# Kernel tuning notes

Hardware: AMD Instinct MI355X
Metric: run time of the kernel (lower is better)

The kernel has to match this reference:

```python
import jax, jax.numpy as jnp
import numpy as np

B, S, D, H, W, L, V = 4, 8192, 256, 8, 64, 6, 256
DH = D // H          # head dim 32
NW = S // W          # number of windows
FF = 4 * D


def setup_inputs() -> dict:
    key = jax.random.key(0)
    ks = jax.random.split(key, 12)
    w = lambda k, shape: (jax.random.normal(k, shape, jnp.float32) * 0.02)
    return {
        "input_ids": jax.random.randint(ks[0], (B, S), 0, V).astype(jnp.int32),
        "attention_mask": jnp.ones((B, S), jnp.int32),
        "word_start": jax.random.randint(ks[1], (B, S), 0, 2).astype(jnp.int32),
        "emb": w(ks[2], (V, D)),
        "pos_emb": w(ks[3], (S, D)),
        "ln1_g": jnp.ones((L, D)), "ln1_b": jnp.zeros((L, D)),
        "wq": w(ks[4], (L, D, D)), "wk": w(ks[5], (L, D, D)),
        "wv": w(ks[6], (L, D, D)), "wo": w(ks[7], (L, D, D)),
        "ln2_g": jnp.ones((L, D)), "ln2_b": jnp.zeros((L, D)),
        "w1": w(ks[8], (L, D, FF)), "b1": jnp.zeros((L, FF)),
        "w2": w(ks[9], (L, FF, D)), "b2": jnp.zeros((L, D)),
        "lnf_g": jnp.ones((D,)), "lnf_b": jnp.zeros((D,)),
    }


def _ln(x, g, b):
    m = jnp.mean(x, -1, keepdims=True)
    v = jnp.mean((x - m) ** 2, -1, keepdims=True)
    return (x - m) * jax.lax.rsqrt(v + 1e-5) * g + b


def _local_attn(x, mask_bool, wq, wk, wv, wo):
    # non-causal local attention: each 64-token window attends to
    # [prev window, own window, next window] (look_backward=1, look_forward=1)
    def heads(t):
        return t.reshape(B, S, H, DH).transpose(0, 2, 1, 3)  # [B,H,S,DH]
    q = heads(x @ wq)
    k = heads(x @ wk)
    v = heads(x @ wv)
    qw = q.reshape(B, H, NW, W, DH)

    def ctx(t):  # gather 3-window key/value context
        tw = t.reshape(B, H, NW, W, DH)
        tp = jnp.pad(tw, ((0, 0), (0, 0), (1, 1), (0, 0), (0, 0)))
        return jnp.concatenate([tp[:, :, i:i + NW] for i in range(3)], axis=3)  # [B,H,NW,3W,DH]

    kc, vc = ctx(k), ctx(v)
    mw = mask_bool.reshape(B, NW, W)
    mp = jnp.pad(mw, ((0, 0), (1, 1), (0, 0)))
    mc = jnp.concatenate([mp[:, i:i + NW] for i in range(3)], axis=2)  # [B,NW,3W]

    scores = jnp.einsum('bhnwd,bhnkd->bhnwk', qw, kc) * (DH ** -0.5)
    scores = jnp.where(mc[:, None, :, None, :], scores, -1e9)
    attn = jax.nn.softmax(scores, axis=-1)
    o = jnp.einsum('bhnwk,bhnkd->bhnwd', attn, vc)
    o = o.reshape(B, H, S, DH).transpose(0, 2, 1, 3).reshape(B, S, D)
    return o @ wo


def _gather_word_starts(x, ws):
    # pack hidden states at word-start positions to the front, zero-padded
    def one(xb, wb):
        idx = jnp.cumsum(wb) - 1
        tgt = jnp.where(wb > 0, idx, S)  # invalid rows go to scratch slot S
        return jnp.zeros((S + 1, xb.shape[-1]), xb.dtype).at[tgt].set(xb)[:S]
    return jax.vmap(one)(x, ws)


def reference(input_ids, attention_mask, word_start, emb, pos_emb,
              ln1_g, ln1_b, wq, wk, wv, wo, ln2_g, ln2_b,
              w1, b1, w2, b2, lnf_g, lnf_b):
    mask_bool = attention_mask > 0
    x = emb[input_ids] + pos_emb[None, :, :]
    for i in range(L):
        x = x + _local_attn(_ln(x, ln1_g[i], ln1_b[i]), mask_bool,
                            wq[i], wk[i], wv[i], wo[i])
        h = _ln(x, ln2_g[i], ln2_b[i])
        x = x + jax.nn.gelu(h @ w1[i] + b1[i]) @ w2[i] + b2[i]
    x = _ln(x, lnf_g, lnf_b)
    return _gather_word_starts(x, word_start)
```

## Files before the change

### kernel.cpp

```cpp
#include <hip/hip_runtime.h>


#define S_LEN 8192
#define BATCH 4
#define DMODEL 256
#define NHEAD 8
#define WIN 64
#define NWIN 128
#define NLAYER 6
#define FFDIM 1024
#define MROWS (BATCH * S_LEN)

typedef float __attribute__((ext_vector_type(4))) f32x4;
typedef unsigned int __attribute__((ext_vector_type(2))) u32x2;
typedef unsigned short u16;
typedef unsigned short __attribute__((ext_vector_type(4))) u16x4;

__device__ __forceinline__ u16 f2bf(float f) {
  unsigned u = __builtin_bit_cast(unsigned, f);
  u += 0x7fffu + ((u >> 16) & 1u);
  return (u16)(u >> 16);
}

__device__ __forceinline__ unsigned cvt_pk_bf16(float lo, float hi) {
  unsigned r;
  asm("v_cvt_pk_bf16_f32 %0, %1, %2" : "=v"(r) : "v"(lo), "v"(hi));
  return r;
}
__device__ __forceinline__ u32x2 pack_bf16x4(f32x4 v) {
  u32x2 o;
  o[0] = cvt_pk_bf16(v[0], v[1]);
  o[1] = cvt_pk_bf16(v[2], v[3]);
  return o;
}

__device__ __forceinline__ void mfma16(f32x4& d, f32x4 a, f32x4 b) {
  asm volatile("v_mfma_f32_16x16x32_bf16 %0, %1, %2, %0"
               : "+v"(d) : "v"(a), "v"(b));
}
#define MFMA_FENCE() asm volatile("s_nop 7\n\ts_nop 7")

__device__ __forceinline__ void gload_lds16(const void* g, void* l) {
  __builtin_amdgcn_global_load_lds(
      (__attribute__((address_space(1))) void*)g,
      (__attribute__((address_space(3))) void*)l, 16, 0, 0);
}

__device__ __forceinline__ float gelu_f(float t) {
  float u = 0.7978845608028654f * (t + 0.044715f * t * t * t);
  float e = __expf(-2.0f * u);
  return t * __builtin_amdgcn_rcpf(1.0f + e);
}

__global__ __launch_bounds__(256) void embed_ln_kernel(
    const int* __restrict__ ids, const float* __restrict__ emb,
    const float* __restrict__ pos, const float* __restrict__ g,
    const float* __restrict__ b, float* __restrict__ x, u16* __restrict__ xb) {
  int wid = threadIdx.x >> 6, lane = threadIdx.x & 63;
  int r = blockIdx.x * 4 + wid;
  int s = r & (S_LEN - 1);
  int id = ids[r];
  f32x4 e = *(const f32x4*)(emb + (size_t)id * DMODEL + lane * 4);
  f32x4 p = *(const f32x4*)(pos + (size_t)s * DMODEL + lane * 4);
  f32x4 v = e + p;
  *(f32x4*)(x + (size_t)r * DMODEL + lane * 4) = v;
  float sm = v[0] + v[1] + v[2] + v[3];
  float q = v[0] * v[0] + v[1] * v[1] + v[2] * v[2] + v[3] * v[3];
  for (int off = 32; off; off >>= 1) {
    sm += __shfl_xor(sm, off, 64);
    q += __shfl_xor(q, off, 64);
  }
  float mean = sm * (1.0f / DMODEL);
  float var = q * (1.0f / DMODEL) - mean * mean;
  float rs = rsqrtf(var + 1e-5f);
  f32x4 gg = *(const f32x4*)(g + lane * 4);
  f32x4 bb = *(const f32x4*)(b + lane * 4);
  f32x4 o;
  for (int j = 0; j < 4; ++j) o[j] = (v[j] - mean) * rs * gg[j] + bb[j];
  *(u32x2*)(xb + (size_t)r * DMODEL + lane * 4) = pack_bf16x4(o);
}

__global__ void zero_kernel(float* __restrict__ p, int n4) {
  int i = blockIdx.x * blockDim.x + threadIdx.x;
  int stride = gridDim.x * blockDim.x;
  f32x4 z = {0.f, 0.f, 0.f, 0.f};
  for (; i < n4; i += stride) ((f32x4*)p)[i] = z;
}

__global__ void tcast_kernel(const float* __restrict__ src, u16* __restrict__ dst,
                             int total, int K, int N, int dls, int rowOff) {
  int i = blockIdx.x * blockDim.x + threadIdx.x;
  int stride = gridDim.x * blockDim.x;
  int KN = K * N;
  for (; i < total; i += stride) {
    int l = i / KN;
    int rem = i - l * KN;
    int k = rem / N;
    int n = rem - k * N;
    dst[l * dls + (rowOff + n) * K + k] = f2bf(src[i]);
  }
}

template <bool GELU_ACT, bool HAS_BIAS>
__global__ __launch_bounds__(256) void gemm_bf16(
    const u16* __restrict__ A, const u16* __restrict__ Bt,
    u16* __restrict__ C, const float* __restrict__ bias,
    int N, int K, int nx) {
  __shared__ u16 As[128 * 64];
  __shared__ u16 Bs[128 * 64];

  int nwg = gridDim.x;
  int bid = blockIdx.x;
  int w8 = (bid & 7) * (nwg >> 3) + (bid >> 3);
  int cx = w8 % nx, ry = w8 / nx;
  int bm = ry * 128, bn = cx * 128;

  int tid = threadIdx.x, lane = tid & 63, wid = tid >> 6;
  int l15 = lane & 15, l4 = lane >> 4;
  int wm = wid >> 1, wn = wid & 1;

  const u16* Ab = A + (size_t)bm * K;
  const u16* Bb = Bt + (size_t)bn * K;

  f32x4 acc[4][4] = {};

  for (int kt = 0; kt < K; kt += 64) {
#pragma unroll
    for (int i = 0; i < 4; ++i) {
      int s = tid + i * 256;
      int r = s >> 3, c = (s & 7) ^ (r & 7);
      gload_lds16(Ab + (size_t)r * K + kt + c * 8,
                  (char*)As + (wid * 64 + i * 256) * 16);
    }
#pragma unroll
    for (int i = 0; i < 4; ++i) {
      int s = tid + i * 256;
      int r = s >> 3, c = (s & 7) ^ (r & 7);
      gload_lds16(Bb + (size_t)r * K + kt + c * 8,
                  (char*)Bs + (wid * 64 + i * 256) * 16);
    }
    __syncthreads();
#pragma unroll
    for (int t = 0; t < 2; ++t) {
      f32x4 af[4], bf[4];
#pragma unroll
      for (int m = 0; m < 4; ++m) {
        int r = wm * 64 + m * 16 + l15;
        af[m] = ((const f32x4*)As)[r * 8 + ((t * 4 + l4) ^ (r & 7))];
      }
#pragma unroll
      for (int n = 0; n < 4; ++n) {
        int r = wn * 64 + n * 16 + l15;
        bf[n] = ((const f32x4*)Bs)[r * 8 + ((t * 4 + l4) ^ (r & 7))];
      }
#pragma unroll
      for (int m = 0; m < 4; ++m)
#pragma unroll
        for (int n = 0; n < 4; ++n) mfma16(acc[m][n], bf[n], af[m]);
    }
    __syncthreads();
  }
  MFMA_FENCE();

  int colB = bn + wn * 64;
  f32x4 bv[4];
#pragma unroll
  for (int n = 0; n < 4; ++n)
    bv[n] = HAS_BIAS ? *(const f32x4*)(bias + colB + n * 16 + l4 * 4)
                     : (f32x4){0.f, 0.f, 0.f, 0.f};
#pragma unroll
  for (int m = 0; m < 4; ++m) {
    int row = bm + wm * 64 + m * 16 + l15;
#pragma unroll
    for (int n = 0; n < 4; ++n) {
      f32x4 v = acc[m][n] + bv[n];
      if (GELU_ACT) {
#pragma unroll
        for (int j = 0; j < 4; ++j) v[j] = gelu_f(v[j]);
      }
      *(u32x2*)(C + (size_t)row * N + colB + n * 16 + l4 * 4) = pack_bf16x4(v);
    }
  }
}

template <bool DO_LN>
__global__ __launch_bounds__(512) void gemm_res_ln(
    const u16* __restrict__ A, const u16* __restrict__ Bt,
    float* __restrict__ x, u16* __restrict__ xb,
    const float* __restrict__ bias, const float* __restrict__ g,
    const float* __restrict__ b, int K) {
  __shared__ u16 As[128 * 64];
  __shared__ u16 Bs[256 * 64];
  __shared__ float redS[128][4];
  __shared__ float redQ[128][4];

  int nwg = gridDim.x;
  int bid = blockIdx.x;
  int bm = ((bid & 7) * (nwg >> 3) + (bid >> 3)) * 128;

  int tid = threadIdx.x, lane = tid & 63, wid = tid >> 6;
  int l15 = lane & 15, l4 = lane >> 4;
  int wm = wid >> 2, wn = wid & 3;

  const u16* Ab = A + (size_t)bm * K;
  f32x4 acc[4][4] = {};

  for (int kt = 0; kt < K; kt += 64) {
#pragma unroll
    for (int i = 0; i < 2; ++i) {
      int s = tid + i * 512;
      int r = s >> 3, c = (s & 7) ^ (r & 7);
      gload_lds16(Ab + (size_t)r * K + kt + c * 8,
                  (char*)As + (wid * 64 + i * 512) * 16);
    }
#pragma unroll
    for (int i = 0; i < 4; ++i) {
      int s = tid + i * 512;
      int r = s >> 3, c = (s & 7) ^ (r & 7);
      gload_lds16(Bt + (size_t)r * K + kt + c * 8,
                  (char*)Bs + (wid * 64 + i * 512) * 16);
    }
    __syncthreads();
#pragma unroll
    for (int t = 0; t < 2; ++t) {
      f32x4 af[4], bf[4];
#pragma unroll
      for (int m = 0; m < 4; ++m) {
        int r = wm * 64 + m * 16 + l15;
        af[m] = ((const f32x4*)As)[r * 8 + ((t * 4 + l4) ^ (r & 7))];
      }
#pragma unroll
      for (int n = 0; n < 4; ++n) {
        int r = wn * 64 + n * 16 + l15;
        bf[n] = ((const f32x4*)Bs)[r * 8 + ((t * 4 + l4) ^ (r & 7))];
      }
#pragma unroll
      for (int m = 0; m < 4; ++m)
#pragma unroll
        for (int n = 0; n < 4; ++n) mfma16(acc[m][n], bf[n], af[m]);
    }
    __syncthreads();
  }
  MFMA_FENCE();

  int colB = wn * 64;
  f32x4 bv[4];
#pragma unroll
  for (int n = 0; n < 4; ++n)
    bv[n] = bias ? *(const f32x4*)(bias + colB + n * 16 + l4 * 4)
                 : (f32x4){0.f, 0.f, 0.f, 0.f};

#pragma unroll
  for (int m = 0; m < 4; ++m) {
    int r = wm * 64 + m * 16 + l15;
    size_t rowoff = (size_t)(bm + r) * DMODEL + colB;
    float s = 0.f, q = 0.f;
#pragma unroll
    for (int n = 0; n < 4; ++n) {
      f32x4 xv = *(const f32x4*)(x + rowoff + n * 16 + l4 * 4);
      f32x4 v = acc[m][n] + bv[n] + xv;
      acc[m][n] = v;
      s += v[0] + v[1] + v[2] + v[3];
      q += v[0] * v[0] + v[1] * v[1] + v[2] * v[2] + v[3] * v[3];
    }
    if (DO_LN) {
      s += __shfl_xor(s, 16, 64);
      s += __shfl_xor(s, 32, 64);
      q += __shfl_xor(q, 16, 64);
      q += __shfl_xor(q, 32, 64);
      if (l4 == 0) {
        redS[r][wn] = s;
        redQ[r][wn] = q;
      }
    }
  }
  if (DO_LN) __syncthreads();

  f32x4 gv[4], bbv[4];
  if (DO_LN) {
#pragma unroll
    for (int n = 0; n < 4; ++n) {
      gv[n] = *(const f32x4*)(g + colB + n * 16 + l4 * 4);
      bbv[n] = *(const f32x4*)(b + colB + n * 16 + l4 * 4);
    }
  }
#pragma unroll
  for (int m = 0; m < 4; ++m) {
    int r = wm * 64 + m * 16 + l15;
    size_t rowoff = (size_t)(bm + r) * DMODEL + colB;
    float mean = 0.f, rs = 0.f;
    if (DO_LN) {
      f32x4 sv = *(const f32x4*)redS[r];
      f32x4 qv = *(const f32x4*)redQ[r];
      float ssum = sv[0] + sv[1] + sv[2] + sv[3];
      float qsum = qv[0] + qv[1] + qv[2] + qv[3];
      mean = ssum * (1.0f / DMODEL);
      float var = qsum * (1.0f / DMODEL) - mean * mean;
      rs = rsqrtf(var + 1e-5f);
    }
#pragma unroll
    for (int n = 0; n < 4; ++n) {
      f32x4 v = acc[m][n];
      *(f32x4*)(x + rowoff + n * 16 + l4 * 4) = v;
      if (DO_LN) {
        f32x4 o;
#pragma unroll
        for (int j = 0; j < 4; ++j)
          o[j] = (v[j] - mean) * rs * gv[n][j] + bbv[n][j];
        *(u32x2*)(xb + rowoff + n * 16 + l4 * 4) = pack_bf16x4(o);
      }
    }
  }
}

__global__ __launch_bounds__(256, 4) void attn_kernel(
    const u16* __restrict__ qkv, const int* __restrict__ amask,
    u16* __restrict__ ao) {
  int win = blockIdx.x, h = blockIdx.y, b = blockIdx.z;
  int tid = threadIdx.x, lane = tid & 63, wid = tid >> 6;
  int l15 = lane & 15, l4 = lane >> 4;

  __shared__ u16 KPs[64 * 216];
  __shared__ u16 Vts[32 * 200];
  __shared__ unsigned char valid[192];

  int t0 = win * WIN - WIN;

  if (tid < 192) {
    int t = t0 + tid;
    valid[tid] = (t >= 0 && t < S_LEN && amask[b * S_LEN + t] != 0) ? 1 : 0;
  }
#pragma unroll
  for (int cc = 0; cc < 3; ++cc) {
    int chunk = cc * 256 + tid;
    int key = chunk >> 2, c = chunk & 3;
    int t = t0 + key;
    t = t < 0 ? 0 : (t >= S_LEN ? S_LEN - 1 : t);
    f32x4 kd = *(const f32x4*)(qkv + (size_t)(b * S_LEN + t) * 768 + 256 + h * 32 + c * 8);
    *(f32x4*)(KPs + key * 40 + c * 8) = kd;
  }
  for (int e = tid; e < 192 * 32; e += 256) {
    int key = e >> 5, d = e & 31;
    int t = t0 + key;
    t = t < 0 ? 0 : (t >= S_LEN ? S_LEN - 1 : t);
    Vts[d * 200 + key] = qkv[(size_t)(b * S_LEN + t) * 768 + 512 + h * 32 + d];
  }
  __syncthreads();

  int qrow = b * S_LEN + win * WIN + wid * 16 + l15;
  f32x4 aq = *(const f32x4*)(qkv + (size_t)qrow * 768 + h * 32 + l4 * 8);

  f32x4 sacc[12] = {};
#pragma unroll
  for (int f = 0; f < 12; ++f) {
    f32x4 bk = *(const f32x4*)(KPs + (f * 16 + l15) * 40 + l4 * 8);
    mfma16(sacc[f], bk, aq);
  }
  MFMA_FENCE();

  const float scale = 0.17677669529663687f;
  float mrow = -1e30f;
#pragma unroll
  for (int f = 0; f < 12; ++f) {
    const unsigned char* vp = &valid[f * 16 + l4 * 4];
#pragma unroll
    for (int j = 0; j < 4; ++j) {
      float sv = vp[j] ? sacc[f][j] * scale : -1e9f;
      sacc[f][j] = sv;
      mrow = fmaxf(mrow, sv);
    }
  }
  mrow = fmaxf(mrow, __shfl_xor(mrow, 16, 64));
  mrow = fmaxf(mrow, __shfl_xor(mrow, 32, 64));

  float ssum = 0.f;
#pragma unroll
  for (int f = 0; f < 12; ++f)
#pragma unroll
    for (int j = 0; j < 4; ++j) {
      float p = __expf(sacc[f][j] - mrow);
      sacc[f][j] = p;
      ssum += p;
    }
  ssum += __shfl_xor(ssum, 16, 64);
  ssum += __shfl_xor(ssum, 32, 64);

  __syncthreads();

#pragma unroll
  for (int f = 0; f < 12; ++f) {
    u32x2 pk;
    pk[0] = cvt_pk_bf16(sacc[f][0], sacc[f][1]);
    pk[1] = cvt_pk_bf16(sacc[f][2], sacc[f][3]);
    *(u32x2*)(KPs + (wid * 16 + l15) * 216 + f * 16 + l4 * 4) = pk;
  }
  __syncthreads();

  f32x4 oacc[2] = {};
#pragma unroll
  for (int kk = 0; kk < 6; ++kk) {
    f32x4 ap = *(const f32x4*)(KPs + (wid * 16 + l15) * 216 + kk * 32 + l4 * 8);
#pragma unroll
    for (int nf = 0; nf < 2; ++nf) {
      f32x4 bvv = *(const f32x4*)(Vts + (nf * 16 + l15) * 200 + kk * 32 + l4 * 8);
      mfma16(oacc[nf], bvv, ap);
    }
  }
  MFMA_FENCE();

  float invv = 1.0f / ssum;
  size_t obase = (size_t)qrow * 256 + h * 32;
#pragma unroll
  for (int nf = 0; nf < 2; ++nf) {
    f32x4 v = oacc[nf] * invv;
    *(u32x2*)(ao + obase + nf * 16 + l4 * 4) = pack_bf16x4(v);
  }
}

__global__ __launch_bounds__(256) void scan_kernel(const int* __restrict__ wsrt,
                                                   int* __restrict__ tgt) {
  __shared__ int part[256];
  int b = blockIdx.x, tid = threadIdx.x;
  const int* src = wsrt + b * S_LEN;
  int* dst = tgt + b * S_LEN;
  int base = tid * 32;
  int loc[32];
  int s = 0;
#pragma unroll
  for (int i = 0; i < 32; ++i) {
    loc[i] = src[base + i];
    s += loc[i];
  }
  part[tid] = s;
  __syncthreads();
  for (int off = 1; off < 256; off <<= 1) {
    int v = (tid >= off) ? part[tid - off] : 0;
    __syncthreads();
    part[tid] += v;
    __syncthreads();
  }
  int cum = part[tid] - s;
#pragma unroll
  for (int i = 0; i < 32; ++i) {
    cum += loc[i];
    dst[base + i] = (loc[i] > 0) ? (cum - 1) : -1;
  }
}

__global__ __launch_bounds__(64) void gather_ln_kernel(
    const float* __restrict__ x, const int* __restrict__ tgt,
    const float* __restrict__ g, const float* __restrict__ b,
    float* __restrict__ out) {
  int r = blockIdx.x;
  int tg = tgt[r];
  if (tg < 0) return;
  int bIdx = r >> 13;
  int lane = threadIdx.x;
  f32x4 v = *(const f32x4*)(x + (size_t)r * DMODEL + lane * 4);
  float s = v[0] + v[1] + v[2] + v[3];
  float q = v[0] * v[0] + v[1] * v[1] + v[2] * v[2] + v[3] * v[3];
  for (int off = 32; off; off >>= 1) {
    s += __shfl_xor(s, off, 64);
    q += __shfl_xor(q, off, 64);
  }
  float mean = s * (1.0f / DMODEL);
  float var = q * (1.0f / DMODEL) - mean * mean;
  float rs = rsqrtf(var + 1e-5f);
  f32x4 gg = *(const f32x4*)(g + lane * 4);
  f32x4 bb = *(const f32x4*)(b + lane * 4);
  f32x4 o;
  for (int j = 0; j < 4; ++j) o[j] = (v[j] - mean) * rs * gg[j] + bb[j];
  *(f32x4*)(out + (size_t)(bIdx * S_LEN + tg) * DMODEL + lane * 4) = o;
}

extern "C" void kernel_launch(void* const* d_in, const int* in_sizes, int n_in,
                              void* d_out, int out_size, void* d_ws,
                              size_t ws_size, hipStream_t stream) {
  const int* ids = (const int*)d_in[0];
  const int* amask = (const int*)d_in[1];
  const int* wstart = (const int*)d_in[2];
  const float* emb = (const float*)d_in[3];
  const float* pos = (const float*)d_in[4];
  const float* ln1g = (const float*)d_in[5];
  const float* ln1b = (const float*)d_in[6];
  const float* wq = (const float*)d_in[7];
  const float* wk = (const float*)d_in[8];
  const float* wv = (const float*)d_in[9];
  const float* wo = (const float*)d_in[10];
  const float* ln2g = (const float*)d_in[11];
  const float* ln2b = (const float*)d_in[12];
  const float* w1 = (const float*)d_in[13];
  const float* b1 = (const float*)d_in[14];
  const float* w2 = (const float*)d_in[15];
  const float* b2 = (const float*)d_in[16];
  const float* lnfg = (const float*)d_in[17];
  const float* lnfb = (const float*)d_in[18];

  char* ws = (char*)d_ws;
  const size_t OFF_X = 0;
  const size_t OFF_XB = 33554432;
  const size_t OFF_AO = 50331648;
  const size_t OFF_BIG = 67108864;
  const size_t OFF_WQKVT = 134217728;
  const size_t OFF_WOT = 136577024;
  const size_t OFF_W1T = 137363456;
  const size_t OFF_W2T = 140509184;
  const size_t OFF_TGT = 143654912;
  const size_t NEEDED = 143785984;
  if (ws_size < NEEDED) return;

  float* x = (float*)(ws + OFF_X);
  u16* xb = (u16*)(ws + OFF_XB);
  u16* ao = (u16*)(ws + OFF_AO);
  u16* big = (u16*)(ws + OFF_BIG);
  u16* WqkvT = (u16*)(ws + OFF_WQKVT);
  u16* WoT = (u16*)(ws + OFF_WOT);
  u16* W1T = (u16*)(ws + OFF_W1T);
  u16* W2T = (u16*)(ws + OFF_W2T);
  int* tgt = (int*)(ws + OFF_TGT);

  tcast_kernel<<<1024, 256, 0, stream>>>(wq, WqkvT, NLAYER * 256 * 256, 256, 256, 768 * 256, 0);
  tcast_kernel<<<1024, 256, 0, stream>>>(wk, WqkvT, NLAYER * 256 * 256, 256, 256, 768 * 256, 256);
  tcast_kernel<<<1024, 256, 0, stream>>>(wv, WqkvT, NLAYER * 256 * 256, 256, 256, 768 * 256, 512);
  tcast_kernel<<<1024, 256, 0, stream>>>(wo, WoT, NLAYER * 256 * 256, 256, 256, 256 * 256, 0);
  tcast_kernel<<<2048, 256, 0, stream>>>(w1, W1T, NLAYER * 256 * 1024, 256, 1024, 1024 * 256, 0);
  tcast_kernel<<<2048, 256, 0, stream>>>(w2, W2T, NLAYER * 1024 * 256, 1024, 256, 256 * 1024, 0);

  embed_ln_kernel<<<MROWS / 4, 256, 0, stream>>>(ids, emb, pos, ln1g, ln1b, x, xb);
  zero_kernel<<<2048, 256, 0, stream>>>((float*)d_out, out_size / 4);
  scan_kernel<<<BATCH, 256, 0, stream>>>(wstart, tgt);

  for (int l = 0; l < NLAYER; ++l) {
    gemm_bf16<false, false><<<1536, 256, 0, stream>>>(
        xb, WqkvT + (size_t)l * 768 * 256, big, nullptr, 768, 256, 6);
    attn_kernel<<<dim3(NWIN, NHEAD, BATCH), 256, 0, stream>>>(big, amask, ao);
    gemm_res_ln<true><<<MROWS / 128, 512, 0, stream>>>(
        ao, WoT + (size_t)l * 256 * 256, x, xb, nullptr,
        ln2g + l * DMODEL, ln2b + l * DMODEL, 256);
    gemm_bf16<true, true><<<2048, 256, 0, stream>>>(
        xb, W1T + (size_t)l * 1024 * 256, big, b1 + l * FFDIM, 1024, 256, 8);
    if (l < NLAYER - 1) {
      gemm_res_ln<true><<<MROWS / 128, 512, 0, stream>>>(
          big, W2T + (size_t)l * 256 * 1024, x, xb, b2 + l * DMODEL,
          ln1g + (l + 1) * DMODEL, ln1b + (l + 1) * DMODEL, 1024);
    } else {
      gemm_res_ln<false><<<MROWS / 128, 512, 0, stream>>>(
          big, W2T + (size_t)l * 256 * 1024, x, nullptr, b2 + l * DMODEL,
          nullptr, nullptr, 1024);
    }
  }

  gather_ln_kernel<<<MROWS, 64, 0, stream>>>(x, tgt, lnfg, lnfb, (float*)d_out);
}
```

Before: 979.4 us.

## Double-buffer GEMM LDS tiles with BK=32 and shrink residual-LN GEMM tiles

Both GEMM kernels now use two LDS buffers with a K-step of 32. The next tile's global-to-LDS load is issued before computing on the current one, and a single vmcnt wait plus barrier replaces the two __syncthreads per iteration. A new 4-column XOR swizzle matches the narrower tile. The residual+LayerNorm GEMM moves from 128-row, 512-thread blocks to 64-row, 256-thread blocks with each wave owning 64 columns, which doubles the grid and lowers LDS per block. In exchange the K loop runs twice as many iterations, each with a barrier, and the smaller tiles reuse data less.

```diff
diff --git a/kernel.cpp b/kernel.cpp
--- a/kernel.cpp
+++ b/kernel.cpp
@@ -40,6 +40,12 @@
 }
 #define MFMA_FENCE() asm volatile("s_nop 7\n\ts_nop 7")
 
+#define PIPE_SYNC()                                      \
+  do {                                                   \
+    asm volatile("s_waitcnt vmcnt(0)" ::: "memory");     \
+    __builtin_amdgcn_s_barrier();                        \
+  } while (0)
+
 __device__ __forceinline__ void gload_lds16(const void* g, void* l) {
   __builtin_amdgcn_global_load_lds(
       (__attribute__((address_space(1))) void*)g,
@@ -51,6 +57,8 @@
   float e = __expf(-2.0f * u);
   return t * __builtin_amdgcn_rcpf(1.0f + e);
 }
+
+__device__ __forceinline__ int swz3(int r) { return (r & 3) ^ ((r >> 2) & 3); }
 
 __global__ __launch_bounds__(256) void embed_ln_kernel(
     const int* __restrict__ ids, const float* __restrict__ emb,
@@ -106,8 +114,8 @@
     const u16* __restrict__ A, const u16* __restrict__ Bt,
     u16* __restrict__ C, const float* __restrict__ bias,
     int N, int K, int nx) {
-  __shared__ u16 As[128 * 64];
-  __shared__ u16 Bs[128 * 64];
+  __shared__ u16 As[2][128 * 32];
+  __shared__ u16 Bs[2][128 * 32];
 
   int nwg = gridDim.x;
   int bid = blockIdx.x;
@@ -123,42 +131,49 @@
   const u16* Bb = Bt + (size_t)bn * K;
 
   f32x4 acc[4][4] = {};
-
-  for (int kt = 0; kt < K; kt += 64) {
-#pragma unroll
-    for (int i = 0; i < 4; ++i) {
+  int NT = K >> 5;
+
+  auto stage = [&](int buf, int kt) {
+#pragma unroll
+    for (int i = 0; i < 2; ++i) {
       int s = tid + i * 256;
-      int r = s >> 3, c = (s & 7) ^ (r & 7);
+      int r = s >> 2, c = (s & 3) ^ swz3(r);
       gload_lds16(Ab + (size_t)r * K + kt + c * 8,
-                  (char*)As + (wid * 64 + i * 256) * 16);
-    }
-#pragma unroll
-    for (int i = 0; i < 4; ++i) {
+                  (char*)As[buf] + (size_t)(i * 256 + wid * 64 + lane) * 16);
+    }
+#pragma unroll
+    for (int i = 0; i < 2; ++i) {
       int s = tid + i * 256;
-      int r = s >> 3, c = (s & 7) ^ (r & 7);
+      int r = s >> 2, c = (s & 3) ^ swz3(r);
       gload_lds16(Bb + (size_t)r * K + kt + c * 8,
-                  (char*)Bs + (wid * 64 + i * 256) * 16);
-    }
-    __syncthreads();
-#pragma unroll
-    for (int t = 0; t < 2; ++t) {
-      f32x4 af[4], bf[4];
-#pragma unroll
-      for (int m = 0; m < 4; ++m) {
-        int r = wm * 64 + m * 16 + l15;
-        af[m] = ((const f32x4*)As)[r * 8 + ((t * 4 + l4) ^ (r & 7))];
-      }
-#pragma unroll
-      for (int n = 0; n < 4; ++n) {
-        int r = wn * 64 + n * 16 + l15;
-        bf[n] = ((const f32x4*)Bs)[r * 8 + ((t * 4 + l4) ^ (r & 7))];
-      }
-#pragma unroll
-      for (int m = 0; m < 4; ++m)
-#pragma unroll
-        for (int n = 0; n < 4; ++n) mfma16(acc[m][n], bf[n], af[m]);
-    }
-    __syncthreads();
+                  (char*)Bs[buf] + (size_t)(i * 256 + wid * 64 + lane) * 16);
+    }
+  };
+
+  stage(0, 0);
+  PIPE_SYNC();
+  int cur = 0;
+  for (int it = 0; it < NT; ++it) {
+    if (it + 1 < NT) stage(cur ^ 1, (it + 1) * 32);
+    const f32x4* Ap = (const f32x4*)As[cur];
+    const f32x4* Bp = (const f32x4*)Bs[cur];
+    f32x4 af[4], bf[4];
+#pragma unroll
+    for (int m = 0; m < 4; ++m) {
+      int r = wm * 64 + m * 16 + l15;
+      af[m] = Ap[r * 4 + (l4 ^ swz3(r))];
+    }
+#pragma unroll
+    for (int n = 0; n < 4; ++n) {
+      int r = wn * 64 + n * 16 + l15;
+      bf[n] = Bp[r * 4 + (l4 ^ swz3(r))];
+    }
+#pragma unroll
+    for (int m = 0; m < 4; ++m)
+#pragma unroll
+      for (int n = 0; n < 4; ++n) mfma16(acc[m][n], bf[n], af[m]);
+    PIPE_SYNC();
+    cur ^= 1;
   }
   MFMA_FENCE();
 
@@ -184,66 +199,71 @@
 }
 
 template <bool DO_LN>
-__global__ __launch_bounds__(512) void gemm_res_ln(
+__global__ __launch_bounds__(256) void gemm_res_ln(
     const u16* __restrict__ A, const u16* __restrict__ Bt,
     float* __restrict__ x, u16* __restrict__ xb,
     const float* __restrict__ bias, const float* __restrict__ g,
     const float* __restrict__ b, int K) {
-  __shared__ u16 As[128 * 64];
-  __shared__ u16 Bs[256 * 64];
-  __shared__ float redS[128][4];
-  __shared__ float redQ[128][4];
+  __shared__ u16 As[2][64 * 32];
+  __shared__ u16 Bs[2][256 * 32];
+  __shared__ float redS[64][4];
+  __shared__ float redQ[64][4];
 
   int nwg = gridDim.x;
   int bid = blockIdx.x;
-  int bm = ((bid & 7) * (nwg >> 3) + (bid >> 3)) * 128;
+  int bm = ((bid & 7) * (nwg >> 3) + (bid >> 3)) * 64;
 
   int tid = threadIdx.x, lane = tid & 63, wid = tid >> 6;
   int l15 = lane & 15, l4 = lane >> 4;
-  int wm = wid >> 2, wn = wid & 3;
 
   const u16* Ab = A + (size_t)bm * K;
   f32x4 acc[4][4] = {};
-
-  for (int kt = 0; kt < K; kt += 64) {
-#pragma unroll
-    for (int i = 0; i < 2; ++i) {
-      int s = tid + i * 512;
-      int r = s >> 3, c = (s & 7) ^ (r & 7);
+  int NT = K >> 5;
+
+  auto stage = [&](int buf, int kt) {
+    {
+      int s = tid;
+      int r = s >> 2, c = (s & 3) ^ swz3(r);
       gload_lds16(Ab + (size_t)r * K + kt + c * 8,
-                  (char*)As + (wid * 64 + i * 512) * 16);
+                  (char*)As[buf] + (size_t)(wid * 64 + lane) * 16);
     }
 #pragma unroll
     for (int i = 0; i < 4; ++i) {
-      int s = tid + i * 512;
-      int r = s >> 3, c = (s & 7) ^ (r & 7);
+      int s = tid + i * 256;
+      int r = s >> 2, c = (s & 3) ^ swz3(r);
       gload_lds16(Bt + (size_t)r * K + kt + c * 8,
-                  (char*)Bs + (wid * 64 + i * 512) * 16);
-    }
-    __syncthreads();
-#pragma unroll
-    for (int t = 0; t < 2; ++t) {
-      f32x4 af[4], bf[4];
-#pragma unroll
-      for (int m = 0; m < 4; ++m) {
-        int r = wm * 64 + m * 16 + l15;
-        af[m] = ((const f32x4*)As)[r * 8 + ((t * 4 + l4) ^ (r & 7))];
-      }
-#pragma unroll
-      for (int n = 0; n < 4; ++n) {
-        int r = wn * 64 + n * 16 + l15;
-        bf[n] = ((const f32x4*)Bs)[r * 8 + ((t * 4 + l4) ^ (r & 7))];
-      }
-#pragma unroll
-      for (int m = 0; m < 4; ++m)
-#pragma unroll
-        for (int n = 0; n < 4; ++n) mfma16(acc[m][n], bf[n], af[m]);
-    }
-    __syncthreads();
+                  (char*)Bs[buf] + (size_t)(i * 256 + wid * 64 + lane) * 16);
+    }
+  };
+
+  stage(0, 0);
+  PIPE_SYNC();
+  int cur = 0;
+  for (int it = 0; it < NT; ++it) {
+    if (it + 1 < NT) stage(cur ^ 1, (it + 1) * 32);
+    const f32x4* Ap = (const f32x4*)As[cur];
+    const f32x4* Bp = (const f32x4*)Bs[cur];
+    f32x4 af[4], bf[4];
+#pragma unroll
+    for (int m = 0; m < 4; ++m) {
+      int r = m * 16 + l15;
+      af[m] = Ap[r * 4 + (l4 ^ swz3(r))];
+    }
+#pragma unroll
+    for (int n = 0; n < 4; ++n) {
+      int r = wid * 64 + n * 16 + l15;
+      bf[n] = Bp[r * 4 + (l4 ^ swz3(r))];
+    }
+#pragma unroll
+    for (int m = 0; m < 4; ++m)
+#pragma unroll
+      for (int n = 0; n < 4; ++n) mfma16(acc[m][n], bf[n], af[m]);
+    PIPE_SYNC();
+    cur ^= 1;
   }
   MFMA_FENCE();
 
-  int colB = wn * 64;
+  int colB = wid * 64;
   f32x4 bv[4];
 #pragma unroll
   for (int n = 0; n < 4; ++n)
@@ -252,7 +272,7 @@
 
 #pragma unroll
   for (int m = 0; m < 4; ++m) {
-    int r = wm * 64 + m * 16 + l15;
+    int r = m * 16 + l15;
     size_t rowoff = (size_t)(bm + r) * DMODEL + colB;
     float s = 0.f, q = 0.f;
 #pragma unroll
@@ -269,8 +289,8 @@
       q += __shfl_xor(q, 16, 64);
       q += __shfl_xor(q, 32, 64);
       if (l4 == 0) {
-        redS[r][wn] = s;
-        redQ[r][wn] = q;
+        redS[r][wid] = s;
+        redQ[r][wid] = q;
       }
     }
   }
@@ -286,7 +306,7 @@
   }
 #pragma unroll
   for (int m = 0; m < 4; ++m) {
-    int r = wm * 64 + m * 16 + l15;
+    int r = m * 16 + l15;
     size_t rowoff = (size_t)(bm + r) * DMODEL + colB;
     float mean = 0.f, rs = 0.f;
     if (DO_LN) {
@@ -534,17 +554,17 @@
     gemm_bf16<false, false><<<1536, 256, 0, stream>>>(
         xb, WqkvT + (size_t)l * 768 * 256, big, nullptr, 768, 256, 6);
     attn_kernel<<<dim3(NWIN, NHEAD, BATCH), 256, 0, stream>>>(big, amask, ao);
-    gemm_res_ln<true><<<MROWS / 128, 512, 0, stream>>>(
+    gemm_res_ln<true><<<MROWS / 64, 256, 0, stream>>>(
         ao, WoT + (size_t)l * 256 * 256, x, xb, nullptr,
         ln2g + l * DMODEL, ln2b + l * DMODEL, 256);
     gemm_bf16<true, true><<<2048, 256, 0, stream>>>(
         xb, W1T + (size_t)l * 1024 * 256, big, b1 + l * FFDIM, 1024, 256, 8);
     if (l < NLAYER - 1) {
-      gemm_res_ln<true><<<MROWS / 128, 512, 0, stream>>>(
+      gemm_res_ln<true><<<MROWS / 64, 256, 0, stream>>>(
           big, W2T + (size_t)l * 256 * 1024, x, xb, b2 + l * DMODEL,
           ln1g + (l + 1) * DMODEL, ln1b + (l + 1) * DMODEL, 1024);
     } else {
-      gemm_res_ln<false><<<MROWS / 128, 512, 0, stream>>>(
+      gemm_res_ln<false><<<MROWS / 64, 256, 0, stream>>>(
           big, W2T + (size_t)l * 256 * 1024, x, nullptr, b2 + l * DMODEL,
           nullptr, nullptr, 1024);
     }
```

New measurement: 1.032 ms. 1.05x slower.
